# Kernel optimization log

Measured on AMD Instinct MI355X. Metric: run time of the kernel, lower is better.

Reference implementation:

```python
import jax, jax.numpy as jnp
import numpy as np
import math

B = 1024
G = 34  # grid_dim = 17*2
C = 4
SCENT = 19


def _scent_kernel_np():
    h = w = SCENT
    mx, my = 0.5 * h, 0.5 * w
    sx, sy = h / 4.0, w / 4.0
    x = np.linspace(0.0, h, h)
    y = np.linspace(0.0, w, w)
    X, Y = np.meshgrid(x, y, indexing='ij')
    z = (1.0 / (2.0 * math.pi * sx * sy)) * np.exp(-(((X - mx) ** 2) / (2 * sx ** 2) + ((Y - my) ** 2) / (2 * sy ** 2)))
    return (z * 80.0).astype(np.float32)


def setup_inputs() -> dict:
    key = jax.random.key(0)
    k1, k2, k3, k4 = jax.random.split(key, 4)
    cell = jax.random.uniform(k1, (B, C, G, G), dtype=jnp.float32)
    food = (jax.random.uniform(k2, (B, G, G), dtype=jnp.float32) > 0.97).astype(jnp.float32)
    fc1_w = jax.random.normal(k3, (64, 12), dtype=jnp.float32) * (1.0 / np.sqrt(12))
    fc1_b = jnp.zeros((64,), dtype=jnp.float32)
    fc2_w = jax.random.normal(k4, (4, 64), dtype=jnp.float32) * (1.0 / np.sqrt(64))
    fc2_b = jnp.zeros((4,), dtype=jnp.float32)
    scent_kernel = jnp.asarray(_scent_kernel_np())
    return {"cell": cell, "food": food, "fc1_w": fc1_w, "fc1_b": fc1_b,
            "fc2_w": fc2_w, "fc2_b": fc2_b, "scent_kernel": scent_kernel, "steps": 32}


def _conv(x, w, pad, groups):
    # x: [B, Cin, H, W], w: [Cout, Cin/groups, kh, kw]; cross-correlation like torch
    return jax.lax.conv_general_dilated(
        x, w, window_strides=(1, 1), padding=[(pad, pad), (pad, pad)],
        feature_group_count=groups, dimension_numbers=('NCHW', 'OIHW', 'NCHW'))


def _maxpool3(x):
    # 3x3 max pool, stride 1, pad 1 (pad value -inf, matching torch MaxPool2d semantics)
    return jax.lax.reduce_window(x, -jnp.inf, jax.lax.max, (1, 1, 3, 3), (1, 1, 1, 1),
                                 [(0, 0), (0, 0), (1, 1), (1, 1)])


def _forward(cell, food, fc1_w, fc1_b, fc2_w, fc2_b, scent_kernel, steps):
    dx = jnp.outer(jnp.array([1., 2., 1.], jnp.float32), jnp.array([-1., 0., 1.], jnp.float32)) / 8.0
    dy = dx.T
    kdx = jnp.tile(dx[None, None], (4, 1, 1, 1))  # depthwise, groups=4
    kdy = jnp.tile(dy[None, None], (4, 1, 1, 1))

    # perceive_scent: 19x19 gaussian conv, padding 9
    scent = _conv(food[:, None], scent_kernel[None, None], 9, 1)[:, 0]  # [B,G,G]

    def step(cell, _):
        cell = cell.at[:, 3].set(scent)
        # current living count per batch (cells in channel 0 above 0.8)
        cl = jnp.sum((cell[:, 0] > 0.8).astype(jnp.float32), axis=(1, 2))
        pre_mask = _maxpool3(cell[:, 0:1]) > 0.1  # [B,1,G,G]
        # perception: x, sobel-x, sobel-y -> 12 channels
        y1 = _conv(cell, kdx, 1, 4)
        y2 = _conv(cell, kdy, 1, 4)
        y = jnp.concatenate([cell, y1, y2], axis=1)  # [B,12,G,G]
        # tiny MLP per pixel (torch transposes dims 1<->3; linear over channels is equivalent)
        h = jax.nn.relu(jnp.einsum('bchw,oc->bohw', y, fc1_w) + fc1_b[None, :, None, None])
        upd = jnp.einsum('bchw,oc->bohw', h, fc2_w) + fc2_b[None, :, None, None]
        x = cell + upd
        post_mask = _maxpool3(x[:, 0:1]) > 0.1
        x = x * (pre_mask & post_mask).astype(x.dtype)
        x = jnp.clip(x, -10.0, 10.0)
        x = x.at[:, 0].set(jnp.clip(x[:, 0], 0.0, 1.0))
        # keep_k_largest: threshold = cl-th smallest (ascending sort index == cl); keep strictly greater
        flat = x[:, 0].reshape(B, -1)  # [B, G*G]
        srt = jnp.sort(flat, axis=1)
        kth = jnp.take_along_axis(srt, cl.astype(jnp.int32)[:, None], axis=1)  # [B,1] (gather clamps OOB)
        flat = jnp.where(flat > kth, flat, 0.0)
        x = x.at[:, 0].set(flat.reshape(B, G, G))
        return x, None

    cell, _ = jax.lax.scan(jax.checkpoint(step), cell, None, length=steps)
    total_pixel_val = cell[:, 0:1].sum(axis=(1, 2, 3))
    living_count = jnp.sum((cell[:, 0:1] > 0.1).astype(jnp.float32), axis=(1, 2, 3))
    return cell, food, total_pixel_val, living_count


def reference(cell, food, fc1_w, fc1_b, fc2_w, fc2_b, scent_kernel, steps):
    return _forward(cell, food, fc1_w, fc1_b, fc2_w, fc2_b, scent_kernel, steps)
```

## Files before the change

### kernel.cpp

```cpp
#include <hip/hip_runtime.h>
#include <stdint.h>

#define GD    34
#define RS    39
#define CBN   (36*RS)
#define NPIX  1156
#define NT    256
#define NB    1024
#define TPR   7
#define TUSED 238
#define FS    57
#define ONEB  0x3f800000u

#define O_C0B 0
#define O_CB1 1404
#define O_CB2 2808
#define O_X0  4212
#define O_HIST 5616
#define POOLN 6704

#define HIDX(bb) ((bb) + ((bb) >> 4))

#define SCAN_PASS(KK) do {                                                         \
    if (wid == 0) {                                                                \
      const int hb = 17 * lane;                                                    \
      int c16[16]; int csum = 0;                                                   \
      _Pragma("unroll")                                                            \
      for (int j = 0; j < 16; ++j) { c16[j] = hist[hb+j]; hist[hb+j] = 0; csum += c16[j]; } \
      int inc2 = csum;                                                             \
      _Pragma("unroll")                                                            \
      for (int off2 = 1; off2 < 64; off2 <<= 1) { int vv = __shfl_up(inc2, off2); if (lane >= off2) inc2 += vv; } \
      const int excl = inc2 - csum;                                                \
      if ((KK) >= excl && (KK) < inc2) {                                           \
        int rem = (KK) - excl; int cum = 0;                                        \
        _Pragma("unroll")                                                          \
        for (int j = 0; j < 16; ++j) {                                             \
          if (rem >= cum && rem < cum + c16[j]) { sel_bin = (lane << 4) + j; sel_rem = rem - cum; } \
          cum += c16[j];                                                           \
        }                                                                          \
      }                                                                            \
    }                                                                              \
  } while (0)

__global__ __launch_bounds__(NT) __attribute__((amdgpu_waves_per_eu(4, 4)))
void ca_kernel(const float* __restrict__ cell_in,
               const float* __restrict__ food_in,
               const float* __restrict__ fc1_w,
               const float* __restrict__ fc1_b,
               const float* __restrict__ fc2_w,
               const float* __restrict__ fc2_b,
               const float* __restrict__ sk_g,
               const int*   __restrict__ steps_p,
               float* __restrict__ out)
{
  __shared__ float pool[POOLN];
  __shared__ unsigned long long avb[2][38];
  __shared__ int   icl[2][4];
  __shared__ int   inzaz[4];
  __shared__ int   ion[4];
  __shared__ int   sel_bin, sel_rem;
  __shared__ float fsum[4];
  __shared__ int   lcnt[4];

  float* c0b  = pool + O_C0B;
  float* cb1  = pool + O_CB1;
  float* cb2  = pool + O_CB2;
  float* x0p  = pool + O_X0;
  int*   hist = (int*)(pool + O_HIST);
  float* foodc = pool;

  const int tid  = threadIdx.x;
  const int b    = blockIdx.x;
  const int lane = tid & 63;
  const int wid  = tid >> 6;
  const int nsteps = steps_p[0];

  const bool tval = (tid < TUSED);
  const int  trow = tval ? (tid / TPR) : 0;
  const int  c0   = tval ? ((tid % TPR) * 5) : 0;
  const int  nval = tval ? ((c0 <= 29) ? 5 : 4) : 0;
  const int  pb1  = (trow+1)*RS + c0 + 1;
  const int  p0   = trow*GD + c0;
  const int  wb   = trow*RS + c0;

  for (int idx = tid; idx < POOLN; idx += NT) pool[idx] = 0.f;
  for (int idx = tid; idx < 76;    idx += NT) ((unsigned long long*)avb)[idx] = 0ull;
  __syncthreads();

#pragma unroll
  for (int j = 0; j < 5; ++j)
    if (j < nval) foodc[(trow+9)*FS + (c0+j+9)] = food_in[(size_t)b*NPIX + p0 + j];
  __syncthreads();

  float scent[5] = {0.f, 0.f, 0.f, 0.f, 0.f};
  for (int dr = 0; dr < 19; ++dr) {
    const float* frow = foodc + (trow+dr)*FS + c0;
    float f[23];
#pragma unroll
    for (int q = 0; q < 23; ++q) f[q] = frow[q];
    const float* krow = sk_g + dr*19;
#pragma unroll
    for (int dc = 0; dc < 19; ++dc) {
      const float kv = krow[dc];
      scent[0] = fmaf(f[dc+0], kv, scent[0]);
      scent[1] = fmaf(f[dc+1], kv, scent[1]);
      scent[2] = fmaf(f[dc+2], kv, scent[2]);
      scent[3] = fmaf(f[dc+3], kv, scent[3]);
      scent[4] = fmaf(f[dc+4], kv, scent[4]);
    }
  }
  __syncthreads();
  for (int idx = tid; idx < O_X0; idx += NT) pool[idx] = 0.f;
  __syncthreads();

  float v3k[5], v1k[5], v2k[5];
  unsigned long long avm0 = 0ull;
  int cnt0 = 0;
#pragma unroll
  for (int j = 0; j < 5; ++j) {
    v3k[j] = 0.f; v1k[j] = 0.f; v2k[j] = 0.f;
    if (j < nval) {
      const float* gi = cell_in + (size_t)b*4*NPIX + p0 + j;
      float v0 = gi[0], v1 = gi[NPIX], v2 = gi[2*NPIX], v3 = gi[3*NPIX];
      c0b[pb1+j] = v0; cb1[pb1+j] = v1; cb2[pb1+j] = v2;
      v3k[j] = v3;
      cnt0 += (v0 > 0.8f) ? 1 : 0;
      if (v0 > 0.1f) avm0 |= (1ull << j);
      x0p[pb1+j] = scent[j];
    }
  }
  if (avm0) atomicOr(&avb[0][trow+2], avm0 << (c0+2));
#pragma unroll
  for (int off = 32; off; off >>= 1) cnt0 += __shfl_down(cnt0, off);
  if (lane == 0) icl[0][wid] = cnt0;
  __syncthreads();
  float sxs[5], sys[5];
#pragma unroll
  for (int j = 0; j < 5; ++j) {
    const int bb = (j < nval) ? (pb1 + j) : pb1;
    float t00=x0p[bb-RS-1], t01=x0p[bb-RS], t02=x0p[bb-RS+1];
    float t10=x0p[bb-1],                    t12=x0p[bb+1];
    float t20=x0p[bb+RS-1], t21=x0p[bb+RS], t22=x0p[bb+RS+1];
    sxs[j] = ((t02 - t00) + 2.f*(t12 - t10) + (t22 - t20)) * 0.125f;
    sys[j] = ((t20 - t00) + 2.f*(t21 - t01) + (t22 - t02)) * 0.125f;
  }

  const float b2r0 = fc2_b[0], b2r1 = fc2_b[1], b2r2 = fc2_b[2], b2r3 = fc2_b[3];

  for (int s = 0; s < nsteps; ++s) {
    __syncthreads();
    const unsigned long long* av = avb[s&1];
    const unsigned long long q0 = av[trow],   q1 = av[trow+1], q2 = av[trow+2],
                             q3 = av[trow+3], q4 = av[trow+4];
    const unsigned long long or3 = q1 | q2 | q3;
    const unsigned long long or5 = or3 | q0 | q4;
    unsigned pm = 0, am = 0;
#pragma unroll
    for (int j = 0; j < 5; ++j) {
      if (j < nval) {
        if ((or3 >> (c0+j+1)) & 7ull)  pm |= (1u << j);
        if ((or5 >> (c0+j))   & 31ull) am |= (1u << j);
      }
    }
    if (__any(am != 0u)) {
      float r0[7], r1[7], r2[7];
#pragma unroll
      for (int q = 0; q < 7; ++q) r0[q] = c0b[wb + q];
#pragma unroll
      for (int q = 0; q < 7; ++q) r1[q] = c0b[wb + RS + q];
#pragma unroll
      for (int q = 0; q < 7; ++q) r2[q] = c0b[wb + 2*RS + q];
#pragma unroll
      for (int j = 0; j < 5; ++j) {
        int acti = (j < nval) ? (int)((am >> j) & 1u) : 0;
        if (__any(acti)) {
          const int bb = pb1 + j;
          const float y0 = r1[j+1];
          const float y4 = ((r0[j+2] - r0[j]) + 2.f*(r1[j+2] - r1[j]) + (r2[j+2] - r2[j])) * 0.125f;
          const float y8 = ((r2[j] - r0[j]) + 2.f*(r2[j+1] - r0[j+1]) + (r2[j+2] - r0[j+2])) * 0.125f;
          float y1, y5, y9, y2, y6, y10;
          {
            const float* cb = cb1;
            float t00=cb[bb-RS-1], t01=cb[bb-RS], t02=cb[bb-RS+1];
            float t10=cb[bb-1],    t11=cb[bb],    t12=cb[bb+1];
            float t20=cb[bb+RS-1], t21=cb[bb+RS], t22=cb[bb+RS+1];
            y1 = t11;
            y5 = ((t02 - t00) + 2.f*(t12 - t10) + (t22 - t20)) * 0.125f;
            y9 = ((t20 - t00) + 2.f*(t21 - t01) + (t22 - t02)) * 0.125f;
          }
          {
            const float* cb = cb2;
            float t00=cb[bb-RS-1], t01=cb[bb-RS], t02=cb[bb-RS+1];
            float t10=cb[bb-1],    t11=cb[bb],    t12=cb[bb+1];
            float t20=cb[bb+RS-1], t21=cb[bb+RS], t22=cb[bb+RS+1];
            y2 = t11;
            y6 = ((t02 - t00) + 2.f*(t12 - t10) + (t22 - t20)) * 0.125f;
            y10= ((t20 - t00) + 2.f*(t21 - t01) + (t22 - t02)) * 0.125f;
          }
          const float y3 = scent[j], y7 = sxs[j], y11 = sys[j];
          float u0 = b2r0, u1 = b2r1, u2 = b2r2, u3 = b2r3;
          for (int o = 0; o < 64; ++o) {
            const float* wr = fc1_w + o*12;
            float t = fc1_b[o];
            t = fmaf(y0, wr[0], t);  t = fmaf(y1, wr[1], t);
            t = fmaf(y2, wr[2], t);  t = fmaf(y3, wr[3], t);
            t = fmaf(y4, wr[4], t);  t = fmaf(y5, wr[5], t);
            t = fmaf(y6, wr[6], t);  t = fmaf(y7, wr[7], t);
            t = fmaf(y8, wr[8], t);  t = fmaf(y9, wr[9], t);
            t = fmaf(y10, wr[10], t); t = fmaf(y11, wr[11], t);
            t = fmaxf(t, 0.f);
            u0 = fmaf(t, fc2_w[o],     u0);
            u1 = fmaf(t, fc2_w[64+o],  u1);
            u2 = fmaf(t, fc2_w[128+o], u2);
            u3 = fmaf(t, fc2_w[192+o], u3);
          }
          v3k[j] = y3 + u3;
          if (j < nval) {
            x0p[bb]  = y0 + u0;
            v1k[j]   = y1 + u1;
            v2k[j]   = y2 + u2;
          }
        }
      }
    }
    __syncthreads();
    if (tid < 38) avb[s&1][tid] = 0ull;
    unsigned pq = 0;
    float midv[5];
#pragma unroll
    for (int j = 0; j < 5; ++j) midv[j] = 0.f;
    if (pm) {
      float dm[7];
#pragma unroll
      for (int jc = 0; jc < 7; ++jc) {
        dm[jc] = 0.f;
        if (jc < nval + 2) {
          const int a = pb1 - 1 + jc;
          float u = x0p[a-RS], m = x0p[a], d = x0p[a+RS];
          dm[jc] = fmaxf(fmaxf(u, m), d);
          if (jc >= 1 && jc <= 5) midv[jc-1] = m;
        }
      }
#pragma unroll
      for (int j = 0; j < 5; ++j)
        if (fmaxf(fmaxf(dm[j], dm[j+1]), dm[j+2]) > 0.1f) pq |= (1u << j);
    }
    int packed = 0, n1c = 0;
    float v0s[5];
#pragma unroll
    for (int j = 0; j < 5; ++j) {
      v0s[j] = 0.f;
      if (j < nval) {
        bool alive = ((pm >> j) & 1u) && ((pq >> j) & 1u);
        float v0 = 0.f, v1 = 0.f, v2 = 0.f, v3 = 0.f;
        if (alive) {
          v0 = fminf(fmaxf(midv[j],   0.f),  1.f);
          v1 = fminf(fmaxf(v1k[j],  -10.f), 10.f);
          v2 = fminf(fmaxf(v2k[j],  -10.f), 10.f);
          v3 = fminf(fmaxf(v3k[j],  -10.f), 10.f);
        }
        cb1[pb1+j] = v1; cb2[pb1+j] = v2; v3k[j] = v3;
        v0s[j] = v0;
        int zer = (v0 == 0.f) ? 1 : 0;
        int azf = (zer && v1 == 0.f && v2 == 0.f && v3 == 0.f) ? 1 : 0;
        packed += zer + (azf << 16);
        n1c += (v0 == 1.0f) ? 1 : 0;
      }
    }
#pragma unroll
    for (int off = 32; off; off >>= 1) {
      packed += __shfl_down(packed, off);
      n1c    += __shfl_down(n1c, off);
    }
    if (lane == 0) { inzaz[wid] = packed; ion[wid] = n1c; }
    __syncthreads();
    const int t01 = inzaz[0]+inzaz[1]+inzaz[2]+inzaz[3];
    const int nz = t01 & 0xffff, az = t01 >> 16;
    const int n1 = ion[0]+ion[1]+ion[2]+ion[3];
    const int ni = NPIX - nz - n1;
    const int cl = icl[s&1][0]+icl[s&1][1]+icl[s&1][2]+icl[s&1][3];
    const int k  = (cl < NPIX) ? cl : (NPIX-1);
    float kth = 0.f;
    if (k >= nz) {
      if (k - nz >= ni) {
        kth = 1.0f;
      } else {
        const int k2 = k - nz;
#pragma unroll
        for (int j = 0; j < 5; ++j) {
          unsigned u = __float_as_uint(v0s[j]);
          if (j < nval && u != 0u && u != ONEB) atomicAdd(&hist[HIDX(u >> 20)], 1);
        }
        __syncthreads();
        SCAN_PASS(k2);
        __syncthreads();
        const int bin1 = sel_bin; const int kr2 = sel_rem;
#pragma unroll
        for (int j = 0; j < 5; ++j) {
          unsigned u = __float_as_uint(v0s[j]);
          if (j < nval && u != 0u && (u >> 20) == (unsigned)bin1)
            atomicAdd(&hist[HIDX((u >> 10) & 1023u)], 1);
        }
        __syncthreads();
        SCAN_PASS(kr2);
        __syncthreads();
        const int bin2 = sel_bin; const int kr3 = sel_rem;
        const unsigned pref2 = (((unsigned)bin1) << 10) | (unsigned)bin2;
#pragma unroll
        for (int j = 0; j < 5; ++j) {
          unsigned u = __float_as_uint(v0s[j]);
          if (j < nval && u != 0u && (u >> 10) == pref2)
            atomicAdd(&hist[HIDX(u & 1023u)], 1);
        }
        __syncthreads();
        SCAN_PASS(kr3);
        __syncthreads();
        kth = __uint_as_float((((unsigned)bin1) << 20) | (((unsigned)bin2) << 10) | (unsigned)sel_bin);
      }
    }
    unsigned long long avm = 0ull;
    int cnt = 0;
#pragma unroll
    for (int j = 0; j < 5; ++j) {
      if (j < nval) {
        float w0 = (v0s[j] > kth) ? v0s[j] : 0.f;
        c0b[pb1+j] = w0;
        cnt += (w0 > 0.8f) ? 1 : 0;
        if (w0 > 0.1f) avm |= (1ull << j);
      }
    }
    if (avm) atomicOr(&avb[(s+1)&1][trow+2], avm << (c0+2));
#pragma unroll
    for (int off = 32; off; off >>= 1) cnt += __shfl_down(cnt, off);
    if (lane == 0) icl[(s+1)&1][wid] = cnt;
    if (az == NPIX) break;
  }

  const size_t CELL_N = (size_t)4*NPIX*NB;
  const size_t FOOD_N = (size_t)NPIX*NB;
  float tp = 0.f; int lcv = 0;
#pragma unroll
  for (int j = 0; j < 5; ++j) {
    if (j < nval) {
      const int p = p0 + j;
      float c0v = c0b[pb1+j], c1 = cb1[pb1+j], c2 = cb2[pb1+j];
      size_t go = (size_t)b*4*NPIX + p;
      out[go]          = c0v;
      out[go +   NPIX] = c1;
      out[go + 2*NPIX] = c2;
      out[go + 3*NPIX] = v3k[j];
      out[CELL_N + (size_t)b*NPIX + p] = food_in[(size_t)b*NPIX + p];
      tp += c0v;
      lcv += (c0v > 0.1f) ? 1 : 0;
    }
  }
#pragma unroll
  for (int off = 32; off; off >>= 1) { tp += __shfl_down(tp, off); lcv += __shfl_down(lcv, off); }
  if (lane == 0) { fsum[wid] = tp; lcnt[wid] = lcv; }
  __syncthreads();
  if (tid == 0) {
    out[CELL_N + FOOD_N + b]      = fsum[0]+fsum[1]+fsum[2]+fsum[3];
    out[CELL_N + FOOD_N + NB + b] = (float)(lcnt[0]+lcnt[1]+lcnt[2]+lcnt[3]);
  }
}

extern "C" void kernel_launch(void* const* d_in, const int* in_sizes, int n_in,
                              void* d_out, int out_size, void* d_ws, size_t ws_size,
                              hipStream_t stream) {
  const float* cell  = (const float*)d_in[0];
  const float* food  = (const float*)d_in[1];
  const float* fc1w  = (const float*)d_in[2];
  const float* fc1b  = (const float*)d_in[3];
  const float* fc2w  = (const float*)d_in[4];
  const float* fc2b  = (const float*)d_in[5];
  const float* sk    = (const float*)d_in[6];
  const int*   steps = (const int*)d_in[7];
  float* out = (float*)d_out;
  ca_kernel<<<NB, NT, 0, stream>>>(cell, food, fc1w, fc1b, fc2w, fc2b, sk, steps, out);
}
```

Before: 226.9 us.

## Compact active pixels across wave lanes before evaluating the per-pixel MLP

Before, each thread looped over its 5 pixels and ran the 64-wide MLP under per-pixel divergence, which left lanes idle wherever only some pixels were active. Now each wave ballots its active pixels, packs them densely across lanes, and every lane runs the MLP for one packed pixel. Scent and gradient inputs are fetched with shuffles, channel 0 gradients come from shared-memory stencils, and results are written to new shared buffers x1p, x2p and x3p. The histogram now aliases x3p, so it gets an explicit zeroing pass and an extra barrier. Shared memory use grows, which may lower occupancy, and the index decoding adds some overhead.

```diff
diff --git a/kernel.cpp b/kernel.cpp
--- a/kernel.cpp
+++ b/kernel.cpp
@@ -3,7 +3,6 @@
 
 #define GD    34
 #define RS    39
-#define CBN   (36*RS)
 #define NPIX  1156
 #define NT    256
 #define NB    1024
@@ -16,8 +15,10 @@
 #define O_CB1 1404
 #define O_CB2 2808
 #define O_X0  4212
-#define O_HIST 5616
-#define POOLN 6704
+#define O_X1  5616
+#define O_X2  6772
+#define O_X3  7928
+#define POOLN 9084
 
 #define HIDX(bb) ((bb) + ((bb) >> 4))
 
@@ -66,7 +67,10 @@
   float* cb1  = pool + O_CB1;
   float* cb2  = pool + O_CB2;
   float* x0p  = pool + O_X0;
-  int*   hist = (int*)(pool + O_HIST);
+  float* x1p  = pool + O_X1;
+  float* x2p  = pool + O_X2;
+  float* x3p  = pool + O_X3;
+  int*   hist = (int*)(pool + O_X3);
   float* foodc = pool;
 
   const int tid  = threadIdx.x;
@@ -81,7 +85,6 @@
   const int  nval = tval ? ((c0 <= 29) ? 5 : 4) : 0;
   const int  pb1  = (trow+1)*RS + c0 + 1;
   const int  p0   = trow*GD + c0;
-  const int  wb   = trow*RS + c0;
 
   for (int idx = tid; idx < POOLN; idx += NT) pool[idx] = 0.f;
   for (int idx = tid; idx < 76;    idx += NT) ((unsigned long long*)avb)[idx] = 0ull;
@@ -113,12 +116,12 @@
   for (int idx = tid; idx < O_X0; idx += NT) pool[idx] = 0.f;
   __syncthreads();
 
-  float v3k[5], v1k[5], v2k[5];
+  float v3k[5];
   unsigned long long avm0 = 0ull;
   int cnt0 = 0;
 #pragma unroll
   for (int j = 0; j < 5; ++j) {
-    v3k[j] = 0.f; v1k[j] = 0.f; v2k[j] = 0.f;
+    v3k[j] = 0.f;
     if (j < nval) {
       const float* gi = cell_in + (size_t)b*4*NPIX + p0 + j;
       float v0 = gi[0], v1 = gi[NPIX], v2 = gi[2*NPIX], v3 = gi[3*NPIX];
@@ -162,42 +165,80 @@
         if ((or5 >> (c0+j))   & 31ull) am |= (1u << j);
       }
     }
-    if (__any(am != 0u)) {
-      float r0[7], r1[7], r2[7];
-#pragma unroll
-      for (int q = 0; q < 7; ++q) r0[q] = c0b[wb + q];
-#pragma unroll
-      for (int q = 0; q < 7; ++q) r1[q] = c0b[wb + RS + q];
-#pragma unroll
-      for (int q = 0; q < 7; ++q) r2[q] = c0b[wb + 2*RS + q];
-#pragma unroll
-      for (int j = 0; j < 5; ++j) {
-        int acti = (j < nval) ? (int)((am >> j) & 1u) : 0;
-        if (__any(acti)) {
-          const int bb = pb1 + j;
-          const float y0 = r1[j+1];
-          const float y4 = ((r0[j+2] - r0[j]) + 2.f*(r1[j+2] - r1[j]) + (r2[j+2] - r2[j])) * 0.125f;
-          const float y8 = ((r2[j] - r0[j]) + 2.f*(r2[j+1] - r0[j+1]) + (r2[j+2] - r0[j+2])) * 0.125f;
-          float y1, y5, y9, y2, y6, y10;
+    {
+      const unsigned long long mk0 = __ballot((am >> 0) & 1u);
+      const unsigned long long mk1 = __ballot((am >> 1) & 1u);
+      const unsigned long long mk2 = __ballot((am >> 2) & 1u);
+      const unsigned long long mk3 = __ballot((am >> 3) & 1u);
+      const unsigned long long mk4 = __ballot((am >> 4) & 1u);
+      const int P0 = __popcll(mk0);
+      const int P1 = P0 + __popcll(mk1);
+      const int P2 = P1 + __popcll(mk2);
+      const int P3 = P2 + __popcll(mk3);
+      const int Ntot = P3 + __popcll(mk4);
+      const int rounds = (Ntot + 63) >> 6;
+      for (int r = 0; r < rounds; ++r) {
+        const int i = (r << 6) + lane;
+        if (i < Ntot) {
+          const int jj = (i >= P0) + (i >= P1) + (i >= P2) + (i >= P3);
+          int base = 0;
+          base = (jj >= 1) ? P0 : base; base = (jj >= 2) ? P1 : base;
+          base = (jj >= 3) ? P2 : base; base = (jj >= 4) ? P3 : base;
+          int tt = i - base;
+          unsigned long long mm = mk0;
+          mm = (jj == 1) ? mk1 : mm; mm = (jj == 2) ? mk2 : mm;
+          mm = (jj == 3) ? mk3 : mm; mm = (jj == 4) ? mk4 : mm;
+          int pos = 0;
+#pragma unroll
+          for (int bb2 = 32; bb2 >= 1; bb2 >>= 1) {
+            int cw = __popcll(mm & (((1ull << bb2) - 1ull) << pos));
+            if (tt >= cw) { tt -= cw; pos += bb2; }
+          }
+          const int ts  = (wid << 6) + pos;
+          const int trw = (ts * 9363) >> 16;
+          const int col = (ts - trw * 7) * 5 + jj;
+          const int p   = trw * GD + col;
+          const int h0  = (trw + 1) * RS + col + 1;
+          float s0v = __shfl(scent[0], pos), s1v = __shfl(scent[1], pos),
+                s2v = __shfl(scent[2], pos), s3v = __shfl(scent[3], pos),
+                s4v = __shfl(scent[4], pos);
+          float a0v = __shfl(sxs[0], pos), a1v = __shfl(sxs[1], pos),
+                a2v = __shfl(sxs[2], pos), a3v = __shfl(sxs[3], pos),
+                a4v = __shfl(sxs[4], pos);
+          float b0v = __shfl(sys[0], pos), b1v = __shfl(sys[1], pos),
+                b2v = __shfl(sys[2], pos), b3v = __shfl(sys[3], pos),
+                b4v = __shfl(sys[4], pos);
+          const float y3  = (jj==0)?s0v:(jj==1)?s1v:(jj==2)?s2v:(jj==3)?s3v:s4v;
+          const float y7  = (jj==0)?a0v:(jj==1)?a1v:(jj==2)?a2v:(jj==3)?a3v:a4v;
+          const float y11 = (jj==0)?b0v:(jj==1)?b1v:(jj==2)?b2v:(jj==3)?b3v:b4v;
+          float y0, y4, y8, y1, y5, y9, y2, y6, y10;
+          {
+            const float* cb = c0b;
+            float t00=cb[h0-RS-1], t01=cb[h0-RS], t02=cb[h0-RS+1];
+            float t10=cb[h0-1],    t11=cb[h0],    t12=cb[h0+1];
+            float t20=cb[h0+RS-1], t21=cb[h0+RS], t22=cb[h0+RS+1];
+            y0 = t11;
+            y4 = ((t02 - t00) + 2.f*(t12 - t10) + (t22 - t20)) * 0.125f;
+            y8 = ((t20 - t00) + 2.f*(t21 - t01) + (t22 - t02)) * 0.125f;
+          }
           {
             const float* cb = cb1;
-            float t00=cb[bb-RS-1], t01=cb[bb-RS], t02=cb[bb-RS+1];
-            float t10=cb[bb-1],    t11=cb[bb],    t12=cb[bb+1];
-            float t20=cb[bb+RS-1], t21=cb[bb+RS], t22=cb[bb+RS+1];
+            float t00=cb[h0-RS-1], t01=cb[h0-RS], t02=cb[h0-RS+1];
+            float t10=cb[h0-1],    t11=cb[h0],    t12=cb[h0+1];
+            float t20=cb[h0+RS-1], t21=cb[h0+RS], t22=cb[h0+RS+1];
             y1 = t11;
             y5 = ((t02 - t00) + 2.f*(t12 - t10) + (t22 - t20)) * 0.125f;
             y9 = ((t20 - t00) + 2.f*(t21 - t01) + (t22 - t02)) * 0.125f;
           }
           {
             const float* cb = cb2;
-            float t00=cb[bb-RS-1], t01=cb[bb-RS], t02=cb[bb-RS+1];
-            float t10=cb[bb-1],    t11=cb[bb],    t12=cb[bb+1];
-            float t20=cb[bb+RS-1], t21=cb[bb+RS], t22=cb[bb+RS+1];
+            float t00=cb[h0-RS-1], t01=cb[h0-RS], t02=cb[h0-RS+1];
+            float t10=cb[h0-1],    t11=cb[h0],    t12=cb[h0+1];
+            float t20=cb[h0+RS-1], t21=cb[h0+RS], t22=cb[h0+RS+1];
             y2 = t11;
             y6 = ((t02 - t00) + 2.f*(t12 - t10) + (t22 - t20)) * 0.125f;
             y10= ((t20 - t00) + 2.f*(t21 - t01) + (t22 - t02)) * 0.125f;
           }
-          const float y3 = scent[j], y7 = sxs[j], y11 = sys[j];
           float u0 = b2r0, u1 = b2r1, u2 = b2r2, u3 = b2r3;
           for (int o = 0; o < 64; ++o) {
             const float* wr = fc1_w + o*12;
@@ -214,12 +255,10 @@
             u2 = fmaf(t, fc2_w[128+o], u2);
             u3 = fmaf(t, fc2_w[192+o], u3);
           }
-          v3k[j] = y3 + u3;
-          if (j < nval) {
-            x0p[bb]  = y0 + u0;
-            v1k[j]   = y1 + u1;
-            v2k[j]   = y2 + u2;
-          }
+          x0p[h0] = y0 + u0;
+          x1p[p]  = y1 + u1;
+          x2p[p]  = y2 + u2;
+          x3p[p]  = y3 + u3;
         }
       }
     }
@@ -254,10 +293,10 @@
         bool alive = ((pm >> j) & 1u) && ((pq >> j) & 1u);
         float v0 = 0.f, v1 = 0.f, v2 = 0.f, v3 = 0.f;
         if (alive) {
-          v0 = fminf(fmaxf(midv[j],   0.f),  1.f);
-          v1 = fminf(fmaxf(v1k[j],  -10.f), 10.f);
-          v2 = fminf(fmaxf(v2k[j],  -10.f), 10.f);
-          v3 = fminf(fmaxf(v3k[j],  -10.f), 10.f);
+          v0 = fminf(fmaxf(midv[j],      0.f),  1.f);
+          v1 = fminf(fmaxf(x1p[p0+j], -10.f), 10.f);
+          v2 = fminf(fmaxf(x2p[p0+j], -10.f), 10.f);
+          v3 = fminf(fmaxf(x3p[p0+j], -10.f), 10.f);
         }
         cb1[pb1+j] = v1; cb2[pb1+j] = v2; v3k[j] = v3;
         v0s[j] = v0;
@@ -285,6 +324,8 @@
       if (k - nz >= ni) {
         kth = 1.0f;
       } else {
+        for (int idx = tid; idx < 1088; idx += NT) hist[idx] = 0;
+        __syncthreads();
         const int k2 = k - nz;
 #pragma unroll
         for (int j = 0; j < 5; ++j) {
```

Measured after the change: 230.8 us. Within noise of the previous version (+1.7%).
